# Performance work log

Measured on AMD Instinct MI355X. Metric: run time of the kernel, lower is better.

## Reference

```python
import jax, jax.numpy as jnp
import numpy as np

N_HEAD, F_IN, F_OUT = 4, 768, 64
BS, N = 4, 2048


def setup_inputs() -> dict:
    key = jax.random.key(0)
    k_h, k_w, k_src, k_dst = jax.random.split(key, 4)
    # xavier_uniform bounds
    lim_w = float(np.sqrt(6.0 / (F_IN + F_OUT)))
    lim_a = float(np.sqrt(6.0 / (F_OUT + 1)))
    return {
        "h": jax.random.normal(k_h, (BS, N, F_IN), dtype=jnp.float32),
        "w": jax.random.uniform(k_w, (N_HEAD, F_IN, F_OUT), jnp.float32, -lim_w, lim_w),
        "a_src": jax.random.uniform(k_src, (N_HEAD, F_OUT, 1), jnp.float32, -lim_a, lim_a),
        "a_dst": jax.random.uniform(k_dst, (N_HEAD, F_OUT, 1), jnp.float32, -lim_a, lim_a),
        "bias": jnp.zeros((F_OUT,), dtype=jnp.float32),
    }


def reference(h, w, a_src, a_dst, bias):
    # h: [b, n, f_in]; w: [h, f_in, f_out]
    h_prime = jnp.einsum("bnf,hfo->bhno", h, w)          # [b, h, n, f_out]
    t = jnp.tanh(h_prime)
    attn_src = jnp.einsum("bhno,ho->bhn", t, a_src[..., 0])  # [b, h, n]
    attn_dst = jnp.einsum("bhno,ho->bhn", t, a_dst[..., 0])  # [b, h, n]
    # broadcast add: attn[b,h,i,j] = src[b,h,i] + dst[b,h,j]
    attn = attn_src[..., :, None] + attn_dst[..., None, :]   # [b, h, n, n]
    attn = jnp.where(attn >= 0, attn, 0.2 * attn)            # leaky_relu(0.2)
    attn = jax.nn.softmax(attn, axis=-1)
    out = jnp.einsum("bhij,bhjo->bhio", attn, h_prime)       # [b, h, n, f_out]
    return out + bias
```

## Files before the change

### kernel.cpp

```cpp
#include <hip/hip_runtime.h>
#include <hip/hip_bf16.h>

#define NHEAD 4
#define FIN   768
#define FOUT  64
#define BSZ   4
#define NSEQ  2048
#define BH    (BSZ*NHEAD)
#define LOG2E 1.44269504088896f

typedef __attribute__((ext_vector_type(8)))  short bf16x8;
typedef __attribute__((ext_vector_type(16))) float f32x16;
typedef __attribute__((ext_vector_type(8)))  unsigned short u16x8;
typedef __attribute__((ext_vector_type(4)))  unsigned short u16x4;
typedef __attribute__((ext_vector_type(4)))  unsigned u32x4;

__device__ __forceinline__ unsigned short f2bf(float f){
  unsigned b = __float_as_uint(f);
  return (unsigned short)((b + 0x7fffu + ((b >> 16) & 1u)) >> 16);
}
__device__ __forceinline__ unsigned fenc(float f){
  unsigned b = __float_as_uint(f);
  return (b & 0x80000000u) ? ~b : (b | 0x80000000u);
}
__device__ __forceinline__ float fdec(unsigned u){
  unsigned b = (u & 0x80000000u) ? (u ^ 0x80000000u) : ~u;
  return __uint_as_float(b);
}
__device__ __forceinline__ float fexp2(float x){
#if __has_builtin(__builtin_amdgcn_exp2f)
  return __builtin_amdgcn_exp2f(x);
#else
  return exp2f(x);
#endif
}
__device__ __forceinline__ unsigned pkbf(float lo, float hi){
#if __has_builtin(__builtin_amdgcn_cvt_pk_bf16_f32)
  typedef __attribute__((ext_vector_type(2))) __bf16 bf2;
  union { bf2 v; unsigned u; } cv;
  cv.v = __builtin_amdgcn_cvt_pk_bf16_f32(lo, hi);
  return cv.u;
#else
  return (unsigned)f2bf(lo) | ((unsigned)f2bf(hi) << 16);
#endif
}

__global__ __launch_bounds__(256) void k_prep_w(
    const float* __restrict__ w, unsigned short* __restrict__ wp,
    unsigned* __restrict__ dmaxe)
{
  if (blockIdx.x == 0 && blockIdx.y == 0 && threadIdx.x < BH)
    dmaxe[threadIdx.x] = 0;
  const int head = blockIdx.x, kt = blockIdx.y;
  #pragma unroll
  for (int p = 0; p < 2; ++p){
    int u = threadIdx.x + p*256;
    int o = u >> 3, c = u & 7;
    u16x8 pk;
    #pragma unroll
    for (int j = 0; j < 8; ++j)
      pk[j] = f2bf(w[((size_t)head*FIN + kt*64 + c*8 + j)*FOUT + o]);
    *(u16x8*)((char*)wp + ((size_t)((head*12 + kt)*64 + o))*128 + (c ^ (o & 7))*16) = pk;
  }
}

__global__ __launch_bounds__(512, 2) void k_hprime(
    const float* __restrict__ h, const unsigned short* __restrict__ wp,
    const float* __restrict__ a_src, const float* __restrict__ a_dst,
    unsigned short* __restrict__ hpz2, float* __restrict__ srcv,
    float* __restrict__ dstv, unsigned* __restrict__ dmaxe)
{
  __shared__ __align__(16) char smem[65536];
  float* psumS = (float*)(smem + 16384);
  float* psumD = (float*)(smem + 16896);
  char*  Tt    = smem + 32768;

  const int tid  = threadIdx.x;
  const int i0a  = blockIdx.x * 64;
  const int jbase = i0a & (NSEQ-1);
  const int head = blockIdx.y;
  const int wave = tid >> 6, lane = tid & 63;
  const int wm = wave & 1, wn = (wave >> 1) & 1, kw = wave >> 2;
  const int l32 = lane & 31, h32 = lane >> 5;

  f32x16 acc = {0,0,0,0,0,0,0,0,0,0,0,0,0,0,0,0};

  const int sr = tid >> 3, sc = tid & 7;
  const float* hA = h + (size_t)(i0a + sr)*FIN + sc*8;
  const char*  wB = (const char*)wp + ((size_t)(head*12*64 + sr))*128 + sc*16;
  const int aslot = (sc ^ (sr & 7)) << 4;

  float4 ra0 = *(const float4*)(hA);
  float4 ra1 = *(const float4*)(hA + 4);
  float4 ra2 = *(const float4*)(hA + 64);
  float4 ra3 = *(const float4*)(hA + 68);
  u16x8  rb0 = *(const u16x8*)(wB);
  u16x8  rb1 = *(const u16x8*)(wB + 8192);

  for (int it = 0; it < 6; ++it){
    char* Ab = smem + (it & 1)*16384;
    char* Bb = smem + 32768 + (it & 1)*16384;
    u16x8 pk0, pk1;
    pk0[0]=f2bf(ra0.x); pk0[1]=f2bf(ra0.y); pk0[2]=f2bf(ra0.z); pk0[3]=f2bf(ra0.w);
    pk0[4]=f2bf(ra1.x); pk0[5]=f2bf(ra1.y); pk0[6]=f2bf(ra1.z); pk0[7]=f2bf(ra1.w);
    pk1[0]=f2bf(ra2.x); pk1[1]=f2bf(ra2.y); pk1[2]=f2bf(ra2.z); pk1[3]=f2bf(ra2.w);
    pk1[4]=f2bf(ra3.x); pk1[5]=f2bf(ra3.y); pk1[6]=f2bf(ra3.z); pk1[7]=f2bf(ra3.w);
    *(u16x8*)(Ab + sr*256 + aslot)        = pk0;
    *(u16x8*)(Ab + sr*256 + 128 + aslot)  = pk1;
    *(u16x8*)(Bb + sr*256 + sc*16)        = rb0;
    *(u16x8*)(Bb + sr*256 + 128 + sc*16)  = rb1;
    __syncthreads();
    if (it < 5){
      const float* an = hA + (it+1)*128;
      ra0 = *(const float4*)(an);      ra1 = *(const float4*)(an + 4);
      ra2 = *(const float4*)(an + 64); ra3 = *(const float4*)(an + 68);
      const char* bn = wB + (size_t)(2*(it+1))*8192;
      rb0 = *(const u16x8*)(bn);       rb1 = *(const u16x8*)(bn + 8192);
    }
    #pragma unroll
    for (int s = 0; s < 4; ++s){
      const int slot = (((s*2 + h32) ^ (l32 & 7)) << 4);
      bf16x8 av = *(const bf16x8*)(Ab + (wm*32 + l32)*256 + kw*128 + slot);
      bf16x8 bv = *(const bf16x8*)(Bb + (wn*32 + l32)*256 + kw*128 + slot);
      acc = __builtin_amdgcn_mfma_f32_32x32x16_bf16(av, bv, acc, 0, 0, 0);
    }
  }

  if (kw == 1) *(f32x16*)(smem + (size_t)((wave & 3)*64 + lane)*64) = acc;
  __syncthreads();
  if (kw == 0){
    acc += *(const f32x16*)(smem + (size_t)((wave & 3)*64 + lane)*64);
    const float as = a_src[head*64 + wn*32 + l32];
    const float ad = a_dst[head*64 + wn*32 + l32];
    #pragma unroll
    for (int rb = 0; rb < 4; ++rb){
      const int jb = wm*32 + rb*8 + h32*4;
      u16x4 c4;
      #pragma unroll
      for (int q = 0; q < 4; ++q){
        const float v = acc[rb*4 + q];
        c4[q] = f2bf(v);
        const float t = tanhf(v);
        float ps = t*as, pd = t*ad;
        ps += __shfl_xor(ps, 1);  ps += __shfl_xor(ps, 2);  ps += __shfl_xor(ps, 4);
        ps += __shfl_xor(ps, 8);  ps += __shfl_xor(ps, 16);
        pd += __shfl_xor(pd, 1);  pd += __shfl_xor(pd, 2);  pd += __shfl_xor(pd, 4);
        pd += __shfl_xor(pd, 8);  pd += __shfl_xor(pd, 16);
        if (l32 == 0){
          psumS[(jb + q)*2 + wn] = ps;
          psumD[(jb + q)*2 + wn] = pd;
        }
      }
      const int orow = wn*32 + l32;
      const int slot = ((jb >> 3) & 7) ^ (orow & 7);
      *(u16x4*)(Tt + orow*128 + slot*16 + (jb & 7)*2) = c4;
    }
  }
  __syncthreads();

  const int bh = (i0a >> 11)*NHEAD + head;
  {
    const int o = tid & 63, c = tid >> 6;
    u16x8 val = *(const u16x8*)(Tt + o*128 + (c ^ (o & 7))*16);
    *(u16x8*)((char*)hpz2 + ((size_t)(bh*256 + (jbase >> 3) + c)*64 + o)*16) = val;
  }
  if (tid < 64){
    float sv = (psumS[tid*2] + psumS[tid*2 + 1]) * LOG2E;
    float dv = (psumD[tid*2] + psumD[tid*2 + 1]) * LOG2E;
    srcv[(size_t)bh*NSEQ + jbase + tid] = sv;
    dstv[(size_t)bh*NSEQ + jbase + tid] = dv;
    float dmx = dv;
    dmx = fmaxf(dmx, __shfl_xor(dmx, 1));  dmx = fmaxf(dmx, __shfl_xor(dmx, 2));
    dmx = fmaxf(dmx, __shfl_xor(dmx, 4));  dmx = fmaxf(dmx, __shfl_xor(dmx, 8));
    dmx = fmaxf(dmx, __shfl_xor(dmx, 16)); dmx = fmaxf(dmx, __shfl_xor(dmx, 32));
    if (tid == 0) atomicMax(&dmaxe[bh], fenc(dmx));
  }
}

__global__ __launch_bounds__(512, 4) void k_attn(
    const unsigned short* __restrict__ hpz2, const float* __restrict__ srcv,
    const float* __restrict__ dstv, const unsigned* __restrict__ dmaxe,
    const float* __restrict__ bias, float* __restrict__ out)
{
  __shared__ __align__(16) char smem[33792];
  float* Lbuf = (float*)(smem + 32768);

  const int tid = threadIdx.x;
  const int i0  = blockIdx.x * 64;
  const int bh  = blockIdx.y;
  const int wave = tid >> 6, lane = tid & 63;
  const int wm = wave & 1, jw = wave >> 1;
  const int l32 = lane & 31, h32 = lane >> 5;

  const float s2  = srcv[(size_t)bh*NSEQ + i0 + wm*32 + l32];
  const float dm2 = fdec(dmaxe[bh]);
  float m2 = s2 + dm2; m2 = fmaxf(m2, 0.2f*m2);
  const float* dst = dstv + (size_t)bh*NSEQ;

  const u16x8* gp = (const u16x8*)((const char*)hpz2 + (size_t)bh*256*64*16);

  bf16x8 ones;
  #pragma unroll
  for (int q = 0; q < 8; ++q) ones[q] = (short)0x3F80;

  f32x16 accO0 = {0,0,0,0,0,0,0,0,0,0,0,0,0,0,0,0};
  f32x16 accO1 = {0,0,0,0,0,0,0,0,0,0,0,0,0,0,0,0};
  f32x16 accL  = {0,0,0,0,0,0,0,0,0,0,0,0,0,0,0,0};

  {
    u16x8 r0 = gp[tid], r1 = gp[tid + 512];
    const int J0 = tid >> 6,         o0 = tid & 63;
    const int J1 = (tid + 512) >> 6, o1 = tid & 63;
    *(u16x8*)(smem + (J0*64 + ((o0 + J0) & 63))*16) = r0;
    *(u16x8*)(smem + (J1*64 + ((o1 + J1) & 63))*16) = r1;
  }
  __syncthreads();

  for (int w = 0; w < 16; ++w){
    char* cur = smem + (w & 1)*16384;
    char* nxt = smem + ((w + 1) & 1)*16384;
    u16x8 r0, r1;
    if (w < 15){
      r0 = gp[(w+1)*1024 + tid];
      r1 = gp[(w+1)*1024 + tid + 512];
    }
    #pragma unroll
    for (int stl = 0; stl < 2; ++stl){
      const int Jl = jw*4 + stl*2 + h32;
      const int j0 = (w*16 + Jl)*8;
      float4 d0 = *(const float4*)(dst + j0);
      float4 d1 = *(const float4*)(dst + j0 + 4);
      float e0,e1,e2,e3,e4,e5,e6,e7, x;
      x = s2 + d0.x; x = fmaxf(x, 0.2f*x); e0 = fexp2(x - m2);
      x = s2 + d0.y; x = fmaxf(x, 0.2f*x); e1 = fexp2(x - m2);
      x = s2 + d0.z; x = fmaxf(x, 0.2f*x); e2 = fexp2(x - m2);
      x = s2 + d0.w; x = fmaxf(x, 0.2f*x); e3 = fexp2(x - m2);
      x = s2 + d1.x; x = fmaxf(x, 0.2f*x); e4 = fexp2(x - m2);
      x = s2 + d1.y; x = fmaxf(x, 0.2f*x); e5 = fexp2(x - m2);
      x = s2 + d1.z; x = fmaxf(x, 0.2f*x); e6 = fexp2(x - m2);
      x = s2 + d1.w; x = fmaxf(x, 0.2f*x); e7 = fexp2(x - m2);
      u32x4 pk;
      pk[0] = pkbf(e0, e1); pk[1] = pkbf(e2, e3);
      pk[2] = pkbf(e4, e5); pk[3] = pkbf(e6, e7);
      const bf16x8 pA = __builtin_bit_cast(bf16x8, pk);
      const bf16x8 bv0 = *(const bf16x8*)(cur + (Jl*64 + ((     l32 + Jl) & 63))*16);
      const bf16x8 bv1 = *(const bf16x8*)(cur + (Jl*64 + ((32 + l32 + Jl) & 63))*16);
      accO0 = __builtin_amdgcn_mfma_f32_32x32x16_bf16(pA, bv0, accO0, 0, 0, 0);
      accO1 = __builtin_amdgcn_mfma_f32_32x32x16_bf16(pA, bv1, accO1, 0, 0, 0);
      accL  = __builtin_amdgcn_mfma_f32_32x32x16_bf16(pA, ones, accL, 0, 0, 0);
    }
    if (w < 15){
      const int J0 = tid >> 6,         o0 = tid & 63;
      const int J1 = (tid + 512) >> 6, o1 = tid & 63;
      *(u16x8*)(nxt + (J0*64 + ((o0 + J0) & 63))*16) = r0;
      *(u16x8*)(nxt + (J1*64 + ((o1 + J1) & 63))*16) = r1;
    }
    __syncthreads();
  }

  if (l32 == 0){
    #pragma unroll
    for (int reg = 0; reg < 16; ++reg){
      const int m = (reg & 3) + 8*(reg >> 2) + 4*h32;
      Lbuf[(wm*4 + jw)*32 + m] = accL[reg];
    }
  }

  const float4 bia = *(const float4*)(bias + (tid & 15)*4);
  #pragma unroll
  for (int ph = 0; ph < 2; ++ph){
    __syncthreads();
    if (wm == ph){
      float* ob = (float*)smem;
      #pragma unroll
      for (int reg = 0; reg < 16; ++reg){
        const int m = (reg & 3) + 8*(reg >> 2) + 4*h32;
        ob[(jw*32 + m)*64 +      l32] = accO0[reg];
        ob[(jw*32 + m)*64 + 32 + l32] = accO1[reg];
      }
    }
    __syncthreads();
    {
      const int i = tid >> 4, o4 = (tid & 15)*4;
      const float* ob = (const float*)smem;
      float4 v0 = *(const float4*)(ob + (0*32 + i)*64 + o4);
      float4 v1 = *(const float4*)(ob + (1*32 + i)*64 + o4);
      float4 v2 = *(const float4*)(ob + (2*32 + i)*64 + o4);
      float4 v3 = *(const float4*)(ob + (3*32 + i)*64 + o4);
      const float l = Lbuf[(ph*4+0)*32 + i] + Lbuf[(ph*4+1)*32 + i]
                    + Lbuf[(ph*4+2)*32 + i] + Lbuf[(ph*4+3)*32 + i];
      const float r = 1.f / l;
      float4 res;
      res.x = (v0.x + v1.x + v2.x + v3.x)*r + bia.x;
      res.y = (v0.y + v1.y + v2.y + v3.y)*r + bia.y;
      res.z = (v0.z + v1.z + v2.z + v3.z)*r + bia.z;
      res.w = (v0.w + v1.w + v2.w + v3.w)*r + bia.w;
      *(float4*)(out + ((size_t)bh*NSEQ + i0 + ph*32 + i)*64 + o4) = res;
    }
  }
}

extern "C" void kernel_launch(void* const* d_in, const int* in_sizes, int n_in,
                              void* d_out, int out_size, void* d_ws, size_t ws_size,
                              hipStream_t stream)
{
  const float* h     = (const float*)d_in[0];
  const float* w     = (const float*)d_in[1];
  const float* a_src = (const float*)d_in[2];
  const float* a_dst = (const float*)d_in[3];
  const float* bias  = (const float*)d_in[4];
  float* out = (float*)d_out;

  char* ws = (char*)d_ws;
  unsigned short* hpz2 = (unsigned short*)ws;
  float* srcv = (float*)(ws + (4u<<20));
  float* dstv = (float*)(ws + (4u<<20) + (128u<<10));
  unsigned short* wp = (unsigned short*)(ws + (4u<<20) + (256u<<10));
  unsigned* dmaxe = (unsigned*)(ws + (4u<<20) + (640u<<10));

  k_prep_w<<<dim3(NHEAD, 12), 256, 0, stream>>>(w, wp, dmaxe);
  k_hprime<<<dim3(NSEQ*BSZ/64, NHEAD), 512, 0, stream>>>(h, wp, a_src, a_dst,
                                                         hpz2, srcv, dstv, dmaxe);
  k_attn<<<dim3(NSEQ/64, BH), 512, 0, stream>>>(hpz2, srcv, dstv, dmaxe, bias, out);
}
```

Measured before the change: 123.0 us.

## Load W panels directly from global, compute softmax sum in VALU, simplify LDS layout

In the projection kernel, the B operand (bf16 weights) is now read straight from global/L2 into registers instead of being staged through LDS. That halves LDS use and raises the occupancy hint from 2 to 4, and the weight prep drops its swizzle to match. The bf16 packing of h now uses the pkbf helper. In the attention kernel, the row-sum of exp is accumulated with scalar adds and one shuffle instead of an extra MFMA against a ones vector. Leaky-relu plus max-subtract is refactored into fmax of two fmas, the LDS rotation swizzle for h' is removed, and occupancy rises to 6. The unswizzled LDS reads may cause bank conflicts, and the global B reads rely on cache hits.

```diff
diff --git a/kernel.cpp b/kernel.cpp
--- a/kernel.cpp
+++ b/kernel.cpp
@@ -60,20 +60,20 @@
     #pragma unroll
     for (int j = 0; j < 8; ++j)
       pk[j] = f2bf(w[((size_t)head*FIN + kt*64 + c*8 + j)*FOUT + o]);
-    *(u16x8*)((char*)wp + ((size_t)((head*12 + kt)*64 + o))*128 + (c ^ (o & 7))*16) = pk;
-  }
-}
-
-__global__ __launch_bounds__(512, 2) void k_hprime(
+    *(u16x8*)((char*)wp + ((size_t)((head*12 + kt)*64 + o))*128 + c*16) = pk;
+  }
+}
+
+__global__ __launch_bounds__(512, 4) void k_hprime(
     const float* __restrict__ h, const unsigned short* __restrict__ wp,
     const float* __restrict__ a_src, const float* __restrict__ a_dst,
     unsigned short* __restrict__ hpz2, float* __restrict__ srcv,
     float* __restrict__ dstv, unsigned* __restrict__ dmaxe)
 {
-  __shared__ __align__(16) char smem[65536];
-  float* psumS = (float*)(smem + 16384);
-  float* psumD = (float*)(smem + 16896);
-  char*  Tt    = smem + 32768;
+  __shared__ __align__(16) char smem[32768];
+  float* psumS = (float*)(smem + 24576);
+  float* psumD = (float*)(smem + 25088);
+  char*  Tt    = smem + 16384;
 
   const int tid  = threadIdx.x;
   const int i0a  = blockIdx.x * 64;
@@ -87,43 +87,44 @@
 
   const int sr = tid >> 3, sc = tid & 7;
   const float* hA = h + (size_t)(i0a + sr)*FIN + sc*8;
-  const char*  wB = (const char*)wp + ((size_t)(head*12*64 + sr))*128 + sc*16;
+  const char* wrow = (const char*)wp
+      + ((size_t)(head*12*64) + wn*32 + l32)*128 + h32*16;
   const int aslot = (sc ^ (sr & 7)) << 4;
 
   float4 ra0 = *(const float4*)(hA);
   float4 ra1 = *(const float4*)(hA + 4);
   float4 ra2 = *(const float4*)(hA + 64);
   float4 ra3 = *(const float4*)(hA + 68);
-  u16x8  rb0 = *(const u16x8*)(wB);
-  u16x8  rb1 = *(const u16x8*)(wB + 8192);
 
   for (int it = 0; it < 6; ++it){
     char* Ab = smem + (it & 1)*16384;
-    char* Bb = smem + 32768 + (it & 1)*16384;
-    u16x8 pk0, pk1;
-    pk0[0]=f2bf(ra0.x); pk0[1]=f2bf(ra0.y); pk0[2]=f2bf(ra0.z); pk0[3]=f2bf(ra0.w);
-    pk0[4]=f2bf(ra1.x); pk0[5]=f2bf(ra1.y); pk0[6]=f2bf(ra1.z); pk0[7]=f2bf(ra1.w);
-    pk1[0]=f2bf(ra2.x); pk1[1]=f2bf(ra2.y); pk1[2]=f2bf(ra2.z); pk1[3]=f2bf(ra2.w);
-    pk1[4]=f2bf(ra3.x); pk1[5]=f2bf(ra3.y); pk1[6]=f2bf(ra3.z); pk1[7]=f2bf(ra3.w);
-    *(u16x8*)(Ab + sr*256 + aslot)        = pk0;
-    *(u16x8*)(Ab + sr*256 + 128 + aslot)  = pk1;
-    *(u16x8*)(Bb + sr*256 + sc*16)        = rb0;
-    *(u16x8*)(Bb + sr*256 + 128 + sc*16)  = rb1;
+    u32x4 pk0, pk1;
+    pk0[0] = pkbf(ra0.x, ra0.y); pk0[1] = pkbf(ra0.z, ra0.w);
+    pk0[2] = pkbf(ra1.x, ra1.y); pk0[3] = pkbf(ra1.z, ra1.w);
+    pk1[0] = pkbf(ra2.x, ra2.y); pk1[1] = pkbf(ra2.z, ra2.w);
+    pk1[2] = pkbf(ra3.x, ra3.y); pk1[3] = pkbf(ra3.z, ra3.w);
+    *(u32x4*)(Ab + sr*256 + aslot)       = pk0;
+    *(u32x4*)(Ab + sr*256 + 128 + aslot) = pk1;
     __syncthreads();
     if (it < 5){
       const float* an = hA + (it+1)*128;
       ra0 = *(const float4*)(an);      ra1 = *(const float4*)(an + 4);
       ra2 = *(const float4*)(an + 64); ra3 = *(const float4*)(an + 68);
-      const char* bn = wB + (size_t)(2*(it+1))*8192;
-      rb0 = *(const u16x8*)(bn);       rb1 = *(const u16x8*)(bn + 8192);
-    }
-    #pragma unroll
-    for (int s = 0; s < 4; ++s){
-      const int slot = (((s*2 + h32) ^ (l32 & 7)) << 4);
-      bf16x8 av = *(const bf16x8*)(Ab + (wm*32 + l32)*256 + kw*128 + slot);
-      bf16x8 bv = *(const bf16x8*)(Bb + (wn*32 + l32)*256 + kw*128 + slot);
-      acc = __builtin_amdgcn_mfma_f32_32x32x16_bf16(av, bv, acc, 0, 0, 0);
-    }
+    }
+    const char* wpan = wrow + (size_t)(2*it + kw)*8192;
+    bf16x8 b0 = *(const bf16x8*)(wpan);
+    bf16x8 b1 = *(const bf16x8*)(wpan + 32);
+    bf16x8 b2 = *(const bf16x8*)(wpan + 64);
+    bf16x8 b3 = *(const bf16x8*)(wpan + 96);
+    const char* abase = Ab + (wm*32 + l32)*256 + kw*128;
+    bf16x8 a0 = *(const bf16x8*)(abase + (((0 + h32) ^ (l32 & 7)) << 4));
+    bf16x8 a1 = *(const bf16x8*)(abase + (((2 + h32) ^ (l32 & 7)) << 4));
+    bf16x8 a2 = *(const bf16x8*)(abase + (((4 + h32) ^ (l32 & 7)) << 4));
+    bf16x8 a3 = *(const bf16x8*)(abase + (((6 + h32) ^ (l32 & 7)) << 4));
+    acc = __builtin_amdgcn_mfma_f32_32x32x16_bf16(a0, b0, acc, 0, 0, 0);
+    acc = __builtin_amdgcn_mfma_f32_32x32x16_bf16(a1, b1, acc, 0, 0, 0);
+    acc = __builtin_amdgcn_mfma_f32_32x32x16_bf16(a2, b2, acc, 0, 0, 0);
+    acc = __builtin_amdgcn_mfma_f32_32x32x16_bf16(a3, b3, acc, 0, 0, 0);
   }
 
   if (kw == 1) *(f32x16*)(smem + (size_t)((wave & 3)*64 + lane)*64) = acc;
@@ -161,7 +162,7 @@
   const int bh = (i0a >> 11)*NHEAD + head;
   {
     const int o = tid & 63, c = tid >> 6;
-    u16x8 val = *(const u16x8*)(Tt + o*128 + (c ^ (o & 7))*16);
+    u16x8 val = *(const u16x8*)(Tt + o*128 + ((c ^ (o & 7)) << 4));
     *(u16x8*)((char*)hpz2 + ((size_t)(bh*256 + (jbase >> 3) + c)*64 + o)*16) = val;
   }
   if (tid < 64){
@@ -177,7 +178,7 @@
   }
 }
 
-__global__ __launch_bounds__(512, 4) void k_attn(
+__global__ __launch_bounds__(512, 6) void k_attn(
     const unsigned short* __restrict__ hpz2, const float* __restrict__ srcv,
     const float* __restrict__ dstv, const unsigned* __restrict__ dmaxe,
     const float* __restrict__ bias, float* __restrict__ out)
@@ -195,25 +196,18 @@
   const float s2  = srcv[(size_t)bh*NSEQ + i0 + wm*32 + l32];
   const float dm2 = fdec(dmaxe[bh]);
   float m2 = s2 + dm2; m2 = fmaxf(m2, 0.2f*m2);
+  const float u_ = s2 - m2;
+  const float v_ = 0.2f*s2 - m2;
   const float* dst = dstv + (size_t)bh*NSEQ;
 
   const u16x8* gp = (const u16x8*)((const char*)hpz2 + (size_t)bh*256*64*16);
-
-  bf16x8 ones;
-  #pragma unroll
-  for (int q = 0; q < 8; ++q) ones[q] = (short)0x3F80;
 
   f32x16 accO0 = {0,0,0,0,0,0,0,0,0,0,0,0,0,0,0,0};
   f32x16 accO1 = {0,0,0,0,0,0,0,0,0,0,0,0,0,0,0,0};
-  f32x16 accL  = {0,0,0,0,0,0,0,0,0,0,0,0,0,0,0,0};
-
-  {
-    u16x8 r0 = gp[tid], r1 = gp[tid + 512];
-    const int J0 = tid >> 6,         o0 = tid & 63;
-    const int J1 = (tid + 512) >> 6, o1 = tid & 63;
-    *(u16x8*)(smem + (J0*64 + ((o0 + J0) & 63))*16) = r0;
-    *(u16x8*)(smem + (J1*64 + ((o1 + J1) & 63))*16) = r1;
-  }
+  float lpart = 0.f;
+
+  *(u16x8*)(smem + tid*16)              = gp[tid];
+  *(u16x8*)(smem + (tid + 512)*16)      = gp[tid + 512];
   __syncthreads();
 
   for (int w = 0; w < 16; ++w){
@@ -230,41 +224,34 @@
       const int j0 = (w*16 + Jl)*8;
       float4 d0 = *(const float4*)(dst + j0);
       float4 d1 = *(const float4*)(dst + j0 + 4);
-      float e0,e1,e2,e3,e4,e5,e6,e7, x;
-      x = s2 + d0.x; x = fmaxf(x, 0.2f*x); e0 = fexp2(x - m2);
-      x = s2 + d0.y; x = fmaxf(x, 0.2f*x); e1 = fexp2(x - m2);
-      x = s2 + d0.z; x = fmaxf(x, 0.2f*x); e2 = fexp2(x - m2);
-      x = s2 + d0.w; x = fmaxf(x, 0.2f*x); e3 = fexp2(x - m2);
-      x = s2 + d1.x; x = fmaxf(x, 0.2f*x); e4 = fexp2(x - m2);
-      x = s2 + d1.y; x = fmaxf(x, 0.2f*x); e5 = fexp2(x - m2);
-      x = s2 + d1.z; x = fmaxf(x, 0.2f*x); e6 = fexp2(x - m2);
-      x = s2 + d1.w; x = fmaxf(x, 0.2f*x); e7 = fexp2(x - m2);
+      float e0,e1,e2,e3,e4,e5,e6,e7;
+      e0 = fexp2(fmaxf(u_ + d0.x, fmaf(0.2f, d0.x, v_)));
+      e1 = fexp2(fmaxf(u_ + d0.y, fmaf(0.2f, d0.y, v_)));
+      e2 = fexp2(fmaxf(u_ + d0.z, fmaf(0.2f, d0.z, v_)));
+      e3 = fexp2(fmaxf(u_ + d0.w, fmaf(0.2f, d0.w, v_)));
+      e4 = fexp2(fmaxf(u_ + d1.x, fmaf(0.2f, d1.x, v_)));
+      e5 = fexp2(fmaxf(u_ + d1.y, fmaf(0.2f, d1.y, v_)));
+      e6 = fexp2(fmaxf(u_ + d1.z, fmaf(0.2f, d1.z, v_)));
+      e7 = fexp2(fmaxf(u_ + d1.w, fmaf(0.2f, d1.w, v_)));
+      lpart += ((e0+e1)+(e2+e3)) + ((e4+e5)+(e6+e7));
       u32x4 pk;
       pk[0] = pkbf(e0, e1); pk[1] = pkbf(e2, e3);
       pk[2] = pkbf(e4, e5); pk[3] = pkbf(e6, e7);
       const bf16x8 pA = __builtin_bit_cast(bf16x8, pk);
-      const bf16x8 bv0 = *(const bf16x8*)(cur + (Jl*64 + ((     l32 + Jl) & 63))*16);
-      const bf16x8 bv1 = *(const bf16x8*)(cur + (Jl*64 + ((32 + l32 + Jl) & 63))*16);
+      const bf16x8 bv0 = *(const bf16x8*)(cur + (Jl*64 +      l32)*16);
+      const bf16x8 bv1 = *(const bf16x8*)(cur + (Jl*64 + 32 + l32)*16);
       accO0 = __builtin_amdgcn_mfma_f32_32x32x16_bf16(pA, bv0, accO0, 0, 0, 0);
       accO1 = __builtin_amdgcn_mfma_f32_32x32x16_bf16(pA, bv1, accO1, 0, 0, 0);
-      accL  = __builtin_amdgcn_mfma_f32_32x32x16_bf16(pA, ones, accL, 0, 0, 0);
     }
     if (w < 15){
-      const int J0 = tid >> 6,         o0 = tid & 63;
-      const int J1 = (tid + 512) >> 6, o1 = tid & 63;
-      *(u16x8*)(nxt + (J0*64 + ((o0 + J0) & 63))*16) = r0;
-      *(u16x8*)(nxt + (J1*64 + ((o1 + J1) & 63))*16) = r1;
+      *(u16x8*)(nxt + tid*16)         = r0;
+      *(u16x8*)(nxt + (tid + 512)*16) = r1;
     }
     __syncthreads();
   }
 
-  if (l32 == 0){
-    #pragma unroll
-    for (int reg = 0; reg < 16; ++reg){
-      const int m = (reg & 3) + 8*(reg >> 2) + 4*h32;
-      Lbuf[(wm*4 + jw)*32 + m] = accL[reg];
-    }
-  }
+  lpart += __shfl_xor(lpart, 32);
+  if (lane < 32) Lbuf[(wm*4 + jw)*32 + l32] = lpart;
 
   const float4 bia = *(const float4*)(bias + (tid & 15)*4);
   #pragma unroll
```

Result: slower. 134.4 us (+9.3%).
